# Optimization experiments

Measured on AMD Instinct MI355X. Metric: run time of the kernel, lower is better.

Reference implementation:

```python
import jax, jax.numpy as jnp
import numpy as np

B = 4096      # batch
D_IN = 512    # input_dim
D = 256       # d_model
T = 424       # n_targets
L = 6         # num_layers
EPS = 1e-5    # torch LayerNorm default


def _ln(x, g, b):
    m = jnp.mean(x, axis=-1, keepdims=True)
    v = jnp.var(x, axis=-1, keepdims=True)
    return (x - m) * jax.lax.rsqrt(v + EPS) * g + b


def setup_inputs() -> dict:
    key = jax.random.key(0)
    ks = iter(jax.random.split(key, 32))
    r = lambda shape, s=0.05: jax.random.normal(next(ks), shape, dtype=jnp.float32) * s
    return {
        'x': jax.random.normal(next(ks), (B, D_IN), dtype=jnp.float32),
        'proj_W': r((4, D // 4, D_IN)), 'proj_b': r((4, D // 4)),
        'attn_in_W': r((L, 3 * D, D)), 'attn_in_b': r((L, 3 * D)),
        'attn_out_W': r((L, D, D)), 'attn_out_b': r((L, D)),
        'ln_g': jnp.ones((L, D), jnp.float32), 'ln_b': jnp.zeros((L, D), jnp.float32),
        'ff_W1': r((L, 4 * D, D)), 'ff_b1': r((L, 4 * D)),
        'ff_W2': r((L, D, 4 * D)), 'ff_b2': r((L, D)),
        'cross_in_W': r((3 * D, D)), 'cross_in_b': r((3 * D,)),
        'cross_out_W': r((D, D)), 'cross_out_b': r((D,)),
        'tp_W1': r((T, D // 2, D)), 'tp_b1': r((T, D // 2)),
        'tp_ln_g': jnp.ones((T, D // 2), jnp.float32), 'tp_ln_b': jnp.zeros((T, D // 2), jnp.float32),
        'tp_W2': r((T, D // 4, D // 2)), 'tp_b2': r((T, D // 4)),
        'tp_W3': r((T, D // 4)), 'tp_b3': r((T,)),
    }


def reference(x, proj_W, proj_b, attn_in_W, attn_in_b, attn_out_W, attn_out_b,
              ln_g, ln_b, ff_W1, ff_b1, ff_W2, ff_b2,
              cross_in_W, cross_in_b, cross_out_W, cross_out_b,
              tp_W1, tp_b1, tp_ln_g, tp_ln_b, tp_W2, tp_b2, tp_W3, tp_b3):
    # 4 feature projections -> concat == reshape of stacked einsum  [B, 4, D/4] -> [B, D]
    h = jnp.einsum('bd,pkd->bpk', x, proj_W) + proj_b
    h = h.reshape(h.shape[0], D)

    # 6 transformer blocks on seq_len=1: softmax over a single key == 1, so
    # MHA(x,x,x) reduces exactly to out_proj(v_proj(x)); dropout = identity (eval).
    for i in range(L):
        Wv, bv = attn_in_W[i, 2 * D:], attn_in_b[i, 2 * D:]
        attn = (h @ Wv.T + bv) @ attn_out_W[i].T + attn_out_b[i]
        h = _ln(h + attn, ln_g[i], ln_b[i])          # same norm instance reused
        ff = jax.nn.gelu(h @ ff_W1[i].T + ff_b1[i], approximate=False) @ ff_W2[i].T + ff_b2[i]
        h = _ln(h + ff, ln_g[i], ln_b[i])

    # cross-target attention, also seq_len=1 -> v/out projections only
    Wv, bv = cross_in_W[2 * D:], cross_in_b[2 * D:]
    h = h + ((h @ Wv.T + bv) @ cross_out_W.T + cross_out_b)

    # 424 per-target MLP heads, batched as grouped GEMMs
    t = jnp.einsum('bd,tkd->btk', h, tp_W1) + tp_b1          # [B, T, 128]
    t = jax.nn.relu(_ln(t, tp_ln_g, tp_ln_b))
    t = jax.nn.relu(jnp.einsum('btk,tmk->btm', t, tp_W2) + tp_b2)  # [B, T, 64]
    out = jnp.einsum('btm,tm->bt', t, tp_W3) + tp_b3         # [B, T]
    return out
```

## Files before the change

kernel.cpp:

```cpp
#include <hip/hip_runtime.h>
#include <stdint.h>

using bf16x8 = __attribute__((ext_vector_type(8))) short;
using f32x4  = __attribute__((ext_vector_type(4))) float;

__device__ __forceinline__ f32x4 mfma16(bf16x8 a, bf16x8 b, f32x4 c) {
  return __builtin_amdgcn_mfma_f32_16x16x32_bf16(a, b, c, 0, 0, 0);
}

__device__ __forceinline__ unsigned short f2b_rne(float f) {
  union { float f; unsigned u; } v; v.f = f;
  unsigned r = v.u + 0x7fffu + ((v.u >> 16) & 1u);
  return (unsigned short)(r >> 16);
}

__device__ __forceinline__ void gload16(const void* g, void* l) {
  __builtin_amdgcn_global_load_lds(
      (const __attribute__((address_space(1))) void*)g,
      (__attribute__((address_space(3))) void*)l, 16, 0, 0);
}

__global__ void f2b_kernel(const float* __restrict__ s, unsigned short* __restrict__ d, int n4) {
  int i = blockIdx.x * 256 + threadIdx.x;
  if (i >= n4) return;
  float4 v = reinterpret_cast<const float4*>(s)[i];
  ushort4 o;
  o.x = f2b_rne(v.x); o.y = f2b_rne(v.y); o.z = f2b_rne(v.z); o.w = f2b_rne(v.w);
  reinterpret_cast<ushort4*>(d)[i] = o;
}

template<int EPI>
__global__ __launch_bounds__(256) void gemm_trunk(
    const unsigned short* __restrict__ A, const unsigned short* __restrict__ W,
    const float* __restrict__ bias, float* __restrict__ hf,
    unsigned short* __restrict__ ybf, const float* __restrict__ gam,
    const float* __restrict__ bet, int K, int Nout) {
  __shared__ char sm[34816];
  __shared__ float red[2][4][16];
  const int tid = threadIdx.x, wid = tid >> 6, lane = tid & 63;
  const int g = lane >> 4, r = lane & 15;
  const int row0 = blockIdx.x << 4;
  const int col0 = blockIdx.y << 8;

  f32x4 acc[4] = {};
  const int nk = K >> 5;

  for (int i = wid; i < 17; i += 4) {
    if (i < 16) gload16(W + (size_t)(col0 + i * 16 + (lane >> 2)) * K + (lane & 3) * 8,
                        sm + i * 1024);
    else        gload16(A + (size_t)(row0 + (lane >> 2)) * K + (lane & 3) * 8,
                        sm + 32768);
  }
  for (int ks = 0; ks < nk; ++ks) {
    const int buf = ks & 1;
    __syncthreads();
    if (ks + 1 < nk) {
      const int nb = buf ^ 1, k0 = (ks + 1) << 5;
      for (int i = wid; i < 17; i += 4) {
        if (i < 16) gload16(W + (size_t)(col0 + i * 16 + (lane >> 2)) * K + k0 + (lane & 3) * 8,
                            sm + nb * 16384 + i * 1024);
        else        gload16(A + (size_t)(row0 + (lane >> 2)) * K + k0 + (lane & 3) * 8,
                            sm + 32768 + nb * 1024);
      }
    }
    bf16x8 a = *reinterpret_cast<const bf16x8*>(sm + 32768 + buf * 1024 + r * 64 + g * 16);
#pragma unroll
    for (int n = 0; n < 4; ++n) {
      bf16x8 b = *reinterpret_cast<const bf16x8*>(sm + buf * 16384 + (wid * 64 + n * 16 + r) * 64 + g * 16);
      acc[n] = mfma16(a, b, acc[n]);
    }
  }

  if (EPI == 0 || EPI == 1) {
#pragma unroll
    for (int n = 0; n < 4; ++n) {
      const int lc = wid * 64 + n * 16 + r;
      const float bv = bias[col0 + lc];
#pragma unroll
      for (int j = 0; j < 4; ++j) {
        const int row = row0 + g * 4 + j;
        float y = acc[n][j] + bv;
        if (EPI == 1) y = 0.5f * y * (1.f + erff(y * 0.70710678118654752f));
        ybf[(size_t)row * Nout + col0 + lc] = f2b_rne(y);
      }
    }
  } else if (EPI == 2 || EPI == 4) {
#pragma unroll
    for (int n = 0; n < 4; ++n) {
      const int lc = wid * 64 + n * 16 + r;
      const float bv = bias[lc];
#pragma unroll
      for (int j = 0; j < 4; ++j) {
        const int row = row0 + g * 4 + j;
        float y = acc[n][j] + bv;
        if (EPI == 4) y += hf[(size_t)row * 256 + lc];
        hf[(size_t)row * 256 + lc]  = y;
        ybf[(size_t)row * 256 + lc] = f2b_rne(y);
      }
    }
  } else {
    float xx[4][4];
    float sum[4] = {0.f, 0.f, 0.f, 0.f}, sq[4] = {0.f, 0.f, 0.f, 0.f};
#pragma unroll
    for (int n = 0; n < 4; ++n) {
      const int lc = wid * 64 + n * 16 + r;
      const float bv = bias[lc];
#pragma unroll
      for (int j = 0; j < 4; ++j) {
        float v = hf[(size_t)(row0 + g * 4 + j) * 256 + lc] + acc[n][j] + bv;
        xx[n][j] = v; sum[j] += v; sq[j] += v * v;
      }
    }
#pragma unroll
    for (int m = 1; m < 16; m <<= 1) {
#pragma unroll
      for (int j = 0; j < 4; ++j) {
        sum[j] += __shfl_xor(sum[j], m, 64);
        sq[j]  += __shfl_xor(sq[j],  m, 64);
      }
    }
    if (r == 0) {
#pragma unroll
      for (int j = 0; j < 4; ++j) { red[0][wid][g * 4 + j] = sum[j]; red[1][wid][g * 4 + j] = sq[j]; }
    }
    __syncthreads();
    float mu[4], rs[4];
#pragma unroll
    for (int j = 0; j < 4; ++j) {
      float ts = red[0][0][g * 4 + j] + red[0][1][g * 4 + j] + red[0][2][g * 4 + j] + red[0][3][g * 4 + j];
      float tq = red[1][0][g * 4 + j] + red[1][1][g * 4 + j] + red[1][2][g * 4 + j] + red[1][3][g * 4 + j];
      float mean = ts * (1.f / 256.f);
      mu[j] = mean;
      rs[j] = rsqrtf(tq * (1.f / 256.f) - mean * mean + 1e-5f);
    }
#pragma unroll
    for (int n = 0; n < 4; ++n) {
      const int lc = wid * 64 + n * 16 + r;
      const float gm = gam[lc], bb = bet[lc];
#pragma unroll
      for (int j = 0; j < 4; ++j) {
        const int row = row0 + g * 4 + j;
        float y = (xx[n][j] - mu[j]) * rs[j] * gm + bb;
        hf[(size_t)row * 256 + lc]  = y;
        ybf[(size_t)row * 256 + lc] = f2b_rne(y);
      }
    }
  }
}

__global__ __launch_bounds__(512, 2) void phase_d2(
    const unsigned short* __restrict__ hbf, const unsigned short* __restrict__ w1b,
    const float* __restrict__ b1, const float* __restrict__ lng, const float* __restrict__ lnb,
    const unsigned short* __restrict__ w2b, const float* __restrict__ b2,
    const float* __restrict__ w3, const float* __restrict__ b3,
    float* __restrict__ out) {
  __shared__ char sm[149504];
  const int tid = threadIdx.x, wid = tid >> 6, lane = tid & 63;
  const int r = lane & 15, hi = lane >> 4;
  const int sw = (r & 7) << 4;
  const int t = blockIdx.y;

  const unsigned short* w1t = w1b + (size_t)t * 32768;
  const unsigned short* w2t = w2b + (size_t)t * 8192;
#pragma unroll
  for (int i = 0; i < 8; ++i) {
    const int id = tid + i * 512;
    const int c = id >> 5, s = id & 31;
    bf16x8 v = *reinterpret_cast<const bf16x8*>(w1t + c * 256 + s * 8);
    *reinterpret_cast<bf16x8*>(sm + c * 512 + ((s * 16) ^ ((c & 7) << 4))) = v;
  }
#pragma unroll
  for (int i = 0; i < 2; ++i) {
    const int id = tid + i * 512;
    const int c = id >> 4, s = id & 15;
    bf16x8 v = *reinterpret_cast<const bf16x8*>(w2t + c * 128 + s * 8);
    *reinterpret_cast<bf16x8*>(sm + 65536 + c * 256 + ((s * 16) ^ ((c & 7) << 4))) = v;
  }
  {
    float v;
    if (tid < 128)      v = b1 [t * 128 + tid];
    else if (tid < 256) v = lng[t * 128 + tid - 128];
    else if (tid < 384) v = lnb[t * 128 + tid - 256];
    else if (tid < 448) v = b2 [t * 64  + tid - 384];
    else                v = w3 [t * 64  + tid - 448];
    reinterpret_cast<float*>(sm + 81920)[tid] = v;
  }
  __syncthreads();

  const float* cb1 = reinterpret_cast<const float*>(sm + 81920);
  const float* cg  = cb1 + 128;
  const float* cbe = cb1 + 256;
  const float* cb2 = cb1 + 384;
  const float* cw3 = cb1 + 448;
  char* t1w = sm + 83968 + wid * 8192;
  const float b3t = b3[t];
  const int token_b0 = blockIdx.x * 1024;

  for (int tile = 0; tile < 2; ++tile) {
    const int B0 = token_b0 + tile * 512 + wid * 64;

    f32x4 acc1[8][4] = {};
    bf16x8 bc[4], bn[4];
#pragma unroll
    for (int bf = 0; bf < 4; ++bf)
      bc[bf] = *reinterpret_cast<const bf16x8*>(hbf + (size_t)(B0 + bf * 16 + r) * 256 + hi * 8);
#pragma unroll
    for (int ks = 0; ks < 8; ++ks) {
      bf16x8 a[8];
#pragma unroll
      for (int cf = 0; cf < 8; ++cf)
        a[cf] = *reinterpret_cast<const bf16x8*>(sm + (cf * 16 + r) * 512 + ((ks * 64 + hi * 16) ^ sw));
      if (ks < 7) {
#pragma unroll
        for (int bf = 0; bf < 4; ++bf)
          bn[bf] = *reinterpret_cast<const bf16x8*>(hbf + (size_t)(B0 + bf * 16 + r) * 256 + (ks + 1) * 32 + hi * 8);
      }
#pragma unroll
      for (int cf = 0; cf < 8; ++cf)
#pragma unroll
        for (int bf = 0; bf < 4; ++bf)
          acc1[cf][bf] = mfma16(a[cf], bc[bf], acc1[cf][bf]);
#pragma unroll
      for (int bf = 0; bf < 4; ++bf) bc[bf] = bn[bf];
    }

#pragma unroll
    for (int cf = 0; cf < 8; ++cf) {
      f32x4 b1v = *reinterpret_cast<const f32x4*>(cb1 + cf * 16 + hi * 4);
#pragma unroll
      for (int bf = 0; bf < 4; ++bf) acc1[cf][bf] += b1v;
    }

    float mu[4], rsd[4];
#pragma unroll
    for (int bf = 0; bf < 4; ++bf) {
      float s = 0.f, s2 = 0.f;
#pragma unroll
      for (int cf = 0; cf < 8; ++cf)
#pragma unroll
        for (int j = 0; j < 4; ++j) { float v = acc1[cf][bf][j]; s += v; s2 += v * v; }
      s  += __shfl_xor(s, 16, 64);  s  += __shfl_xor(s, 32, 64);
      s2 += __shfl_xor(s2, 16, 64); s2 += __shfl_xor(s2, 32, 64);
      const float m = s * (1.f / 128.f);
      mu[bf] = m;
      rsd[bf] = rsqrtf(s2 * (1.f / 128.f) - m * m + 1e-5f);
    }

    f32x4 acc2[4][4] = {};
#pragma unroll
    for (int half = 0; half < 2; ++half) {
#pragma unroll
      for (int cf = 0; cf < 8; ++cf) {
        f32x4 gv = *reinterpret_cast<const f32x4*>(cg  + cf * 16 + hi * 4);
        f32x4 bv = *reinterpret_cast<const f32x4*>(cbe + cf * 16 + hi * 4);
#pragma unroll
        for (int bl = 0; bl < 2; ++bl) {
          const int bf = half * 2 + bl;
          unsigned o01, o23;
          {
            float y0 = fmaxf((acc1[cf][bf][0] - mu[bf]) * rsd[bf] * gv[0] + bv[0], 0.f);
            float y1 = fmaxf((acc1[cf][bf][1] - mu[bf]) * rsd[bf] * gv[1] + bv[1], 0.f);
            float y2 = fmaxf((acc1[cf][bf][2] - mu[bf]) * rsd[bf] * gv[2] + bv[2], 0.f);
            float y3 = fmaxf((acc1[cf][bf][3] - mu[bf]) * rsd[bf] * gv[3] + bv[3], 0.f);
            o01 = (unsigned)f2b_rne(y0) | ((unsigned)f2b_rne(y1) << 16);
            o23 = (unsigned)f2b_rne(y2) | ((unsigned)f2b_rne(y3) << 16);
          }
          uint2 pk; pk.x = o01; pk.y = o23;
          *reinterpret_cast<uint2*>(t1w + (bl * 16 + r) * 256 + ((cf * 32 + hi * 8) ^ sw)) = pk;
        }
      }
#pragma unroll
      for (int ks = 0; ks < 4; ++ks) {
        bf16x8 a2[4];
#pragma unroll
        for (int cf2 = 0; cf2 < 4; ++cf2)
          a2[cf2] = *reinterpret_cast<const bf16x8*>(sm + 65536 + (cf2 * 16 + r) * 256 + ((ks * 64 + hi * 16) ^ sw));
#pragma unroll
        for (int bl = 0; bl < 2; ++bl) {
          bf16x8 bb = *reinterpret_cast<const bf16x8*>(t1w + (bl * 16 + r) * 256 + ((ks * 64 + hi * 16) ^ sw));
#pragma unroll
          for (int cf2 = 0; cf2 < 4; ++cf2)
            acc2[cf2][half * 2 + bl] = mfma16(a2[cf2], bb, acc2[cf2][half * 2 + bl]);
        }
      }
    }

    float s[4] = {0.f, 0.f, 0.f, 0.f};
#pragma unroll
    for (int cf2 = 0; cf2 < 4; ++cf2) {
      f32x4 b2v = *reinterpret_cast<const f32x4*>(cb2 + cf2 * 16 + hi * 4);
      f32x4 w3v = *reinterpret_cast<const f32x4*>(cw3 + cf2 * 16 + hi * 4);
#pragma unroll
      for (int bf = 0; bf < 4; ++bf)
#pragma unroll
        for (int j = 0; j < 4; ++j)
          s[bf] += fmaxf(acc2[cf2][bf][j] + b2v[j], 0.f) * w3v[j];
    }
#pragma unroll
    for (int bf = 0; bf < 4; ++bf) {
      s[bf] += __shfl_xor(s[bf], 16, 64);
      s[bf] += __shfl_xor(s[bf], 32, 64);
      if (hi == 0) out[(size_t)(B0 + bf * 16 + r) * 424 + t] = s[bf] + b3t;
    }
  }
}

extern "C" void kernel_launch(void* const* d_in, const int* in_sizes, int n_in,
                              void* d_out, int out_size, void* d_ws, size_t ws_size,
                              hipStream_t stream) {
  const float* x     = (const float*)d_in[0];
  const float* projW = (const float*)d_in[1];
  const float* projb = (const float*)d_in[2];
  const float* aiW   = (const float*)d_in[3];
  const float* aib   = (const float*)d_in[4];
  const float* aoW   = (const float*)d_in[5];
  const float* aob   = (const float*)d_in[6];
  const float* lng   = (const float*)d_in[7];
  const float* lnbp  = (const float*)d_in[8];
  const float* f1W   = (const float*)d_in[9];
  const float* f1b   = (const float*)d_in[10];
  const float* f2W   = (const float*)d_in[11];
  const float* f2bp  = (const float*)d_in[12];
  const float* ciW   = (const float*)d_in[13];
  const float* cib   = (const float*)d_in[14];
  const float* coW   = (const float*)d_in[15];
  const float* cob   = (const float*)d_in[16];
  const float* tpW1  = (const float*)d_in[17];
  const float* tpb1  = (const float*)d_in[18];
  const float* tplng = (const float*)d_in[19];
  const float* tplnb = (const float*)d_in[20];
  const float* tpW2  = (const float*)d_in[21];
  const float* tpb2  = (const float*)d_in[22];
  const float* tpW3  = (const float*)d_in[23];
  const float* tpb3  = (const float*)d_in[24];
  float* out = (float*)d_out;

  char* ws = (char*)d_ws;
  size_t off = 0;
  auto alloc = [&](size_t n) { char* p = ws + off; off = (off + n + 255) & ~(size_t)255; return p; };
  unsigned short* xb   = (unsigned short*)alloc(4096ull * 512 * 2);
  unsigned short* pWb  = (unsigned short*)alloc(256ull * 512 * 2);
  unsigned short* aiWb = (unsigned short*)alloc(6ull * 768 * 256 * 2);
  unsigned short* aoWb = (unsigned short*)alloc(6ull * 256 * 256 * 2);
  unsigned short* f1Wb = (unsigned short*)alloc(6ull * 1024 * 256 * 2);
  unsigned short* f2Wb = (unsigned short*)alloc(6ull * 256 * 1024 * 2);
  unsigned short* ciWb = (unsigned short*)alloc(768ull * 256 * 2);
  unsigned short* coWb = (unsigned short*)alloc(256ull * 256 * 2);
  unsigned short* W1b  = (unsigned short*)alloc(424ull * 128 * 256 * 2);
  unsigned short* W2b  = (unsigned short*)alloc(424ull * 64 * 128 * 2);
  float*          hf   = (float*)alloc(4096ull * 256 * 4);
  unsigned short* hbf  = (unsigned short*)alloc(4096ull * 256 * 2);
  unsigned short* vbf  = (unsigned short*)alloc(4096ull * 256 * 2);
  unsigned short* gbf  = (unsigned short*)alloc(4096ull * 1024 * 2);

  auto conv = [&](const float* s, unsigned short* d, size_t n) {
    int n4 = (int)(n >> 2);
    f2b_kernel<<<dim3((n4 + 255) / 256), dim3(256), 0, stream>>>(s, d, n4);
  };
  conv(x, xb, 4096ull * 512);
  conv(projW, pWb, 256ull * 512);
  conv(aiW, aiWb, 6ull * 768 * 256);
  conv(aoW, aoWb, 6ull * 256 * 256);
  conv(f1W, f1Wb, 6ull * 1024 * 256);
  conv(f2W, f2Wb, 6ull * 256 * 1024);
  conv(ciW, ciWb, 768ull * 256);
  conv(coW, coWb, 256ull * 256);
  conv(tpW1, W1b, 424ull * 128 * 256);
  conv(tpW2, W2b, 424ull * 64 * 128);

  dim3 blk(256);
  gemm_trunk<2><<<dim3(256, 1), blk, 0, stream>>>(xb, pWb, projb, hf, hbf, nullptr, nullptr, 512, 256);
  for (int i = 0; i < 6; ++i) {
    gemm_trunk<0><<<dim3(256, 1), blk, 0, stream>>>(hbf, aiWb + ((size_t)i * 768 + 512) * 256,
                                                    aib + i * 768 + 512, nullptr, vbf, nullptr, nullptr, 256, 256);
    gemm_trunk<3><<<dim3(256, 1), blk, 0, stream>>>(vbf, aoWb + (size_t)i * 256 * 256, aob + i * 256,
                                                    hf, hbf, lng + i * 256, lnbp + i * 256, 256, 256);
    gemm_trunk<1><<<dim3(256, 4), blk, 0, stream>>>(hbf, f1Wb + (size_t)i * 1024 * 256, f1b + i * 1024,
                                                    nullptr, gbf, nullptr, nullptr, 256, 1024);
    gemm_trunk<3><<<dim3(256, 1), blk, 0, stream>>>(gbf, f2Wb + (size_t)i * 256 * 1024, f2bp + i * 256,
                                                    hf, hbf, lng + i * 256, lnbp + i * 256, 1024, 256);
  }
  gemm_trunk<0><<<dim3(256, 1), blk, 0, stream>>>(hbf, ciWb + 512ull * 256, cib + 512,
                                                  nullptr, vbf, nullptr, nullptr, 256, 256);
  gemm_trunk<4><<<dim3(256, 1), blk, 0, stream>>>(vbf, coWb, cob, hf, hbf, nullptr, nullptr, 256, 256);

  phase_d2<<<dim3(4, 424), dim3(512), 0, stream>>>(hbf, W1b, tpb1, tplng, tplnb, W2b, tpb2, tpW3, tpb3, out);
}
```

Before: 599.4 us.

## Fold V and output projections into one weight, restructure trunk GEMM, add MFMA priority

Precomputes Wo·Wv and the combined bias for each attention block and for the cross block, so each of the seven V-projection plus out-projection GEMM pairs becomes a single GEMM and the vbf intermediate disappears. The trunk GEMM is rewritten to stage the A tile into swizzled LDS once and stream weights straight from global memory into registers, with templated row tiles and K. s_setprio is also wrapped around the MFMA bursts in the head kernel. The weight-composition kernel adds per-call fp32 work and rounds the product to bf16 once, which changes numerics slightly compared with rounding the two matrices separately.

```diff
diff --git a/kernel.cpp b/kernel.cpp
--- a/kernel.cpp
+++ b/kernel.cpp
@@ -12,12 +12,6 @@
   union { float f; unsigned u; } v; v.f = f;
   unsigned r = v.u + 0x7fffu + ((v.u >> 16) & 1u);
   return (unsigned short)(r >> 16);
-}
-
-__device__ __forceinline__ void gload16(const void* g, void* l) {
-  __builtin_amdgcn_global_load_lds(
-      (const __attribute__((address_space(1))) void*)g,
-      (__attribute__((address_space(3))) void*)l, 16, 0, 0);
 }
 
 __global__ void f2b_kernel(const float* __restrict__ s, unsigned short* __restrict__ d, int n4) {
@@ -29,86 +23,133 @@
   reinterpret_cast<ushort4*>(d)[i] = o;
 }
 
-template<int EPI>
-__global__ __launch_bounds__(256) void gemm_trunk(
+__global__ __launch_bounds__(256) void compose_attn(
+    const float* __restrict__ aiW, const float* __restrict__ aib,
+    const float* __restrict__ aoW, const float* __restrict__ aob,
+    const float* __restrict__ ciW, const float* __restrict__ cib,
+    const float* __restrict__ coW, const float* __restrict__ cob,
+    unsigned short* __restrict__ wEff, float* __restrict__ bEff) {
+  const int mat = blockIdx.y;
+  const float* Wo = (mat < 6) ? aoW + (size_t)mat * 65536 : coW;
+  const float* Wv = (mat < 6) ? aiW + (size_t)mat * 196608 + 131072 : ciW + 131072;
+  const float* bv = (mat < 6) ? aib + mat * 768 + 512 : cib + 512;
+  const float* bo = (mat < 6) ? aob + mat * 256 : cob;
+  unsigned short* Wd = wEff + (size_t)mat * 65536;
+  const int m = blockIdx.x * 16 + (threadIdx.x >> 4);
+  const int k0 = (threadIdx.x & 15) * 16;
+  float c[16] = {};
+  for (int j = 0; j < 256; ++j) {
+    const float a = Wo[m * 256 + j];
+    const float* Br = Wv + j * 256 + k0;
+#pragma unroll
+    for (int kk = 0; kk < 16; ++kk) c[kk] = fmaf(a, Br[kk], c[kk]);
+  }
+#pragma unroll
+  for (int kk = 0; kk < 16; ++kk) Wd[m * 256 + k0 + kk] = f2b_rne(c[kk]);
+  if (blockIdx.x == 0) {
+    const int mm = threadIdx.x;
+    float s = 0.f;
+    for (int j = 0; j < 256; ++j) s = fmaf(Wo[mm * 256 + j], bv[j], s);
+    bEff[mat * 256 + mm] = s + bo[mm];
+  }
+}
+
+template<int EPI, int ROWS, int K>
+__global__ __launch_bounds__(256, 4) void gemm_t2(
     const unsigned short* __restrict__ A, const unsigned short* __restrict__ W,
     const float* __restrict__ bias, float* __restrict__ hf,
     unsigned short* __restrict__ ybf, const float* __restrict__ gam,
-    const float* __restrict__ bet, int K, int Nout) {
-  __shared__ char sm[34816];
+    const float* __restrict__ bet, int Nout) {
+  constexpr int NBF = ROWS / 16;
+  constexpr int NCF = (ROWS == 16) ? 4 : 2;
+  constexpr int NK = K / 32;
+  constexpr int K2 = K * 2;
+  __shared__ char smA[ROWS * K2];
   __shared__ float red[2][4][16];
   const int tid = threadIdx.x, wid = tid >> 6, lane = tid & 63;
-  const int g = lane >> 4, r = lane & 15;
-  const int row0 = blockIdx.x << 4;
-  const int col0 = blockIdx.y << 8;
-
-  f32x4 acc[4] = {};
-  const int nk = K >> 5;
-
-  for (int i = wid; i < 17; i += 4) {
-    if (i < 16) gload16(W + (size_t)(col0 + i * 16 + (lane >> 2)) * K + (lane & 3) * 8,
-                        sm + i * 1024);
-    else        gload16(A + (size_t)(row0 + (lane >> 2)) * K + (lane & 3) * 8,
-                        sm + 32768);
-  }
-  for (int ks = 0; ks < nk; ++ks) {
-    const int buf = ks & 1;
-    __syncthreads();
-    if (ks + 1 < nk) {
-      const int nb = buf ^ 1, k0 = (ks + 1) << 5;
-      for (int i = wid; i < 17; i += 4) {
-        if (i < 16) gload16(W + (size_t)(col0 + i * 16 + (lane >> 2)) * K + k0 + (lane & 3) * 8,
-                            sm + nb * 16384 + i * 1024);
-        else        gload16(A + (size_t)(row0 + (lane >> 2)) * K + k0 + (lane & 3) * 8,
-                            sm + 32768 + nb * 1024);
-      }
-    }
-    bf16x8 a = *reinterpret_cast<const bf16x8*>(sm + 32768 + buf * 1024 + r * 64 + g * 16);
-#pragma unroll
-    for (int n = 0; n < 4; ++n) {
-      bf16x8 b = *reinterpret_cast<const bf16x8*>(sm + buf * 16384 + (wid * 64 + n * 16 + r) * 64 + g * 16);
-      acc[n] = mfma16(a, b, acc[n]);
-    }
-  }
-
-  if (EPI == 0 || EPI == 1) {
-#pragma unroll
-    for (int n = 0; n < 4; ++n) {
-      const int lc = wid * 64 + n * 16 + r;
-      const float bv = bias[col0 + lc];
-#pragma unroll
-      for (int j = 0; j < 4; ++j) {
-        const int row = row0 + g * 4 + j;
-        float y = acc[n][j] + bv;
-        if (EPI == 1) y = 0.5f * y * (1.f + erff(y * 0.70710678118654752f));
-        ybf[(size_t)row * Nout + col0 + lc] = f2b_rne(y);
-      }
-    }
+  const int r = lane & 15, hi = lane >> 4;
+  const int row0 = blockIdx.x * ROWS;
+  const int colW0 = ((ROWS == 16) ? 0 : blockIdx.y * 128) + wid * (NCF * 16);
+
+  constexpr int CHUNKS = ROWS * K / 8;
+  constexpr int CPR = K / 8;
+#pragma unroll
+  for (int id = tid; id < CHUNKS; id += 256) {
+    const int row = id / CPR, c8 = id % CPR;
+    bf16x8 v = *reinterpret_cast<const bf16x8*>(A + (size_t)(row0 + row) * K + c8 * 8);
+    *reinterpret_cast<bf16x8*>(smA + row * K2 + ((c8 * 16) ^ ((row & 7) << 4))) = v;
+  }
+  __syncthreads();
+
+  const unsigned short* Wb = W + (size_t)(colW0 + r) * K + hi * 8;
+  f32x4 acc[NBF][NCF] = {};
+  bf16x8 wc[NCF], wn[NCF];
+#pragma unroll
+  for (int cf = 0; cf < NCF; ++cf)
+    wc[cf] = *reinterpret_cast<const bf16x8*>(Wb + cf * 16 * K);
+#pragma unroll 4
+  for (int ks = 0; ks < NK; ++ks) {
+    if (ks + 1 < NK) {
+#pragma unroll
+      for (int cf = 0; cf < NCF; ++cf)
+        wn[cf] = *reinterpret_cast<const bf16x8*>(Wb + cf * 16 * K + (ks + 1) * 32);
+    }
+    bf16x8 av[NBF];
+#pragma unroll
+    for (int bf = 0; bf < NBF; ++bf)
+      av[bf] = *reinterpret_cast<const bf16x8*>(
+          smA + (bf * 16 + r) * K2 + ((ks * 64 + hi * 16) ^ ((r & 7) << 4)));
+#pragma unroll
+    for (int bf = 0; bf < NBF; ++bf)
+#pragma unroll
+      for (int cf = 0; cf < NCF; ++cf)
+        acc[bf][cf] = mfma16(av[bf], wc[cf], acc[bf][cf]);
+#pragma unroll
+    for (int cf = 0; cf < NCF; ++cf) wc[cf] = wn[cf];
+  }
+
+  if (EPI == 1) {
+#pragma unroll
+    for (int bf = 0; bf < NBF; ++bf)
+#pragma unroll
+      for (int cf = 0; cf < NCF; ++cf) {
+        const int col = colW0 + cf * 16 + r;
+        const float bv = bias[col];
+#pragma unroll
+        for (int j = 0; j < 4; ++j) {
+          const int row = row0 + bf * 16 + hi * 4 + j;
+          float y = acc[bf][cf][j] + bv;
+          y = 0.5f * y * (1.f + erff(y * 0.70710678118654752f));
+          ybf[(size_t)row * Nout + col] = f2b_rne(y);
+        }
+      }
   } else if (EPI == 2 || EPI == 4) {
 #pragma unroll
-    for (int n = 0; n < 4; ++n) {
-      const int lc = wid * 64 + n * 16 + r;
-      const float bv = bias[lc];
-#pragma unroll
-      for (int j = 0; j < 4; ++j) {
-        const int row = row0 + g * 4 + j;
-        float y = acc[n][j] + bv;
-        if (EPI == 4) y += hf[(size_t)row * 256 + lc];
-        hf[(size_t)row * 256 + lc]  = y;
-        ybf[(size_t)row * 256 + lc] = f2b_rne(y);
-      }
-    }
+    for (int bf = 0; bf < NBF; ++bf)
+#pragma unroll
+      for (int cf = 0; cf < NCF; ++cf) {
+        const int col = colW0 + cf * 16 + r;
+        const float bv = bias[col];
+#pragma unroll
+        for (int j = 0; j < 4; ++j) {
+          const int row = row0 + bf * 16 + hi * 4 + j;
+          float y = acc[bf][cf][j] + bv;
+          if (EPI == 4) y += hf[(size_t)row * 256 + col];
+          hf[(size_t)row * 256 + col]  = y;
+          ybf[(size_t)row * 256 + col] = f2b_rne(y);
+        }
+      }
   } else {
     float xx[4][4];
     float sum[4] = {0.f, 0.f, 0.f, 0.f}, sq[4] = {0.f, 0.f, 0.f, 0.f};
 #pragma unroll
-    for (int n = 0; n < 4; ++n) {
-      const int lc = wid * 64 + n * 16 + r;
-      const float bv = bias[lc];
+    for (int cf = 0; cf < 4; ++cf) {
+      const int col = colW0 + cf * 16 + r;
+      const float bv = bias[col];
 #pragma unroll
       for (int j = 0; j < 4; ++j) {
-        float v = hf[(size_t)(row0 + g * 4 + j) * 256 + lc] + acc[n][j] + bv;
-        xx[n][j] = v; sum[j] += v; sq[j] += v * v;
+        float v = hf[(size_t)(row0 + hi * 4 + j) * 256 + col] + acc[0][cf][j] + bv;
+        xx[cf][j] = v; sum[j] += v; sq[j] += v * v;
       }
     }
 #pragma unroll
@@ -121,28 +162,29 @@
     }
     if (r == 0) {
 #pragma unroll
-      for (int j = 0; j < 4; ++j) { red[0][wid][g * 4 + j] = sum[j]; red[1][wid][g * 4 + j] = sq[j]; }
+      for (int j = 0; j < 4; ++j) { red[0][wid][hi * 4 + j] = sum[j]; red[1][wid][hi * 4 + j] = sq[j]; }
     }
     __syncthreads();
     float mu[4], rs[4];
 #pragma unroll
     for (int j = 0; j < 4; ++j) {
-      float ts = red[0][0][g * 4 + j] + red[0][1][g * 4 + j] + red[0][2][g * 4 + j] + red[0][3][g * 4 + j];
-      float tq = red[1][0][g * 4 + j] + red[1][1][g * 4 + j] + red[1][2][g * 4 + j] + red[1][3][g * 4 + j];
+      const int rr = hi * 4 + j;
+      float ts = red[0][0][rr] + red[0][1][rr] + red[0][2][rr] + red[0][3][rr];
+      float tq = red[1][0][rr] + red[1][1][rr] + red[1][2][rr] + red[1][3][rr];
       float mean = ts * (1.f / 256.f);
       mu[j] = mean;
       rs[j] = rsqrtf(tq * (1.f / 256.f) - mean * mean + 1e-5f);
     }
 #pragma unroll
-    for (int n = 0; n < 4; ++n) {
-      const int lc = wid * 64 + n * 16 + r;
-      const float gm = gam[lc], bb = bet[lc];
+    for (int cf = 0; cf < 4; ++cf) {
+      const int col = colW0 + cf * 16 + r;
+      const float gm = gam[col], bb = bet[col];
 #pragma unroll
       for (int j = 0; j < 4; ++j) {
-        const int row = row0 + g * 4 + j;
-        float y = (xx[n][j] - mu[j]) * rs[j] * gm + bb;
-        hf[(size_t)row * 256 + lc]  = y;
-        ybf[(size_t)row * 256 + lc] = f2b_rne(y);
+        const int row = row0 + hi * 4 + j;
+        float y = (xx[cf][j] - mu[j]) * rs[j] * gm + bb;
+        hf[(size_t)row * 256 + col]  = y;
+        ybf[(size_t)row * 256 + col] = f2b_rne(y);
       }
     }
   }
@@ -215,11 +257,13 @@
         for (int bf = 0; bf < 4; ++bf)
           bn[bf] = *reinterpret_cast<const bf16x8*>(hbf + (size_t)(B0 + bf * 16 + r) * 256 + (ks + 1) * 32 + hi * 8);
       }
+      __builtin_amdgcn_s_setprio(1);
 #pragma unroll
       for (int cf = 0; cf < 8; ++cf)
 #pragma unroll
         for (int bf = 0; bf < 4; ++bf)
           acc1[cf][bf] = mfma16(a[cf], bc[bf], acc1[cf][bf]);
+      __builtin_amdgcn_s_setprio(0);
 #pragma unroll
       for (int bf = 0; bf < 4; ++bf) bc[bf] = bn[bf];
     }
@@ -275,6 +319,7 @@
 #pragma unroll
         for (int cf2 = 0; cf2 < 4; ++cf2)
           a2[cf2] = *reinterpret_cast<const bf16x8*>(sm + 65536 + (cf2 * 16 + r) * 256 + ((ks * 64 + hi * 16) ^ sw));
+        __builtin_amdgcn_s_setprio(1);
 #pragma unroll
         for (int bl = 0; bl < 2; ++bl) {
           bf16x8 bb = *reinterpret_cast<const bf16x8*>(t1w + (bl * 16 + r) * 256 + ((ks * 64 + hi * 16) ^ sw));
@@ -282,6 +327,7 @@
           for (int cf2 = 0; cf2 < 4; ++cf2)
             acc2[cf2][half * 2 + bl] = mfma16(a2[cf2], bb, acc2[cf2][half * 2 + bl]);
         }
+        __builtin_amdgcn_s_setprio(0);
       }
     }
 
@@ -340,49 +386,40 @@
   auto alloc = [&](size_t n) { char* p = ws + off; off = (off + n + 255) & ~(size_t)255; return p; };
   unsigned short* xb   = (unsigned short*)alloc(4096ull * 512 * 2);
   unsigned short* pWb  = (unsigned short*)alloc(256ull * 512 * 2);
-  unsigned short* aiWb = (unsigned short*)alloc(6ull * 768 * 256 * 2);
-  unsigned short* aoWb = (unsigned short*)alloc(6ull * 256 * 256 * 2);
   unsigned short* f1Wb = (unsigned short*)alloc(6ull * 1024 * 256 * 2);
   unsigned short* f2Wb = (unsigned short*)alloc(6ull * 256 * 1024 * 2);
-  unsigned short* ciWb = (unsigned short*)alloc(768ull * 256 * 2);
-  unsigned short* coWb = (unsigned short*)alloc(256ull * 256 * 2);
   unsigned short* W1b  = (unsigned short*)alloc(424ull * 128 * 256 * 2);
   unsigned short* W2b  = (unsigned short*)alloc(424ull * 64 * 128 * 2);
+  unsigned short* wEff = (unsigned short*)alloc(7ull * 256 * 256 * 2);
+  float*          bEff = (float*)alloc(7ull * 256 * 4);
   float*          hf   = (float*)alloc(4096ull * 256 * 4);
   unsigned short* hbf  = (unsigned short*)alloc(4096ull * 256 * 2);
-  unsigned short* vbf  = (unsigned short*)alloc(4096ull * 256 * 2);
   unsigned short* gbf  = (unsigned short*)alloc(4096ull * 1024 * 2);
 
   auto conv = [&](const float* s, unsigned short* d, size_t n) {
     int n4 = (int)(n >> 2);
     f2b_kernel<<<dim3((n4 + 255) / 256), dim3(256), 0, stream>>>(s, d, n4);
   };
+  compose_attn<<<dim3(16, 7), dim3(256), 0, stream>>>(aiW, aib, aoW, aob, ciW, cib, coW, cob, wEff, bEff);
   conv(x, xb, 4096ull * 512);
   conv(projW, pWb, 256ull * 512);
-  conv(aiW, aiWb, 6ull * 768 * 256);
-  conv(aoW, aoWb, 6ull * 256 * 256);
   conv(f1W, f1Wb, 6ull * 1024 * 256);
   conv(f2W, f2Wb, 6ull * 256 * 1024);
-  conv(ciW, ciWb, 768ull * 256);
-  conv(coW, coWb, 256ull * 256);
   conv(tpW1, W1b, 424ull * 128 * 256);
   conv(tpW2, W2b, 424ull * 64 * 128);
 
   dim3 blk(256);
-  gemm_trunk<2><<<dim3(256, 1), blk, 0, stream>>>(xb, pWb, projb, hf, hbf, nullptr, nullptr, 512, 256);
+  gemm_t2<2, 32, 512><<<dim3(128, 2), blk, 0, stream>>>(xb, pWb, projb, hf, hbf, nullptr, nullptr, 256);
   for (int i = 0; i < 6; ++i) {
-    gemm_trunk<0><<<dim3(256, 1), blk, 0, stream>>>(hbf, aiWb + ((size_t)i * 768 + 512) * 256,
-                                                    aib + i * 768 + 512, nullptr, vbf, nullptr, nullptr, 256, 256);
-    gemm_trunk<3><<<dim3(256, 1), blk, 0, stream>>>(vbf, aoWb + (size_t)i * 256 * 256, aob + i * 256,
-                                                    hf, hbf, lng + i * 256, lnbp + i * 256, 256, 256);
-    gemm_trunk<1><<<dim3(256, 4), blk, 0, stream>>>(hbf, f1Wb + (size_t)i * 1024 * 256, f1b + i * 1024,
-                                                    nullptr, gbf, nullptr, nullptr, 256, 1024);
-    gemm_trunk<3><<<dim3(256, 1), blk, 0, stream>>>(gbf, f2Wb + (size_t)i * 256 * 1024, f2bp + i * 256,
-                                                    hf, hbf, lng + i * 256, lnbp + i * 256, 1024, 256);
-  }
-  gemm_trunk<0><<<dim3(256, 1), blk, 0, stream>>>(hbf, ciWb + 512ull * 256, cib + 512,
-                                                  nullptr, vbf, nullptr, nullptr, 256, 256);
-  gemm_trunk<4><<<dim3(256, 1), blk, 0, stream>>>(vbf, coWb, cob, hf, hbf, nullptr, nullptr, 256, 256);
+    gemm_t2<3, 16, 256><<<dim3(256, 1), blk, 0, stream>>>(hbf, wEff + (size_t)i * 65536, bEff + i * 256,
+                                                          hf, hbf, lng + i * 256, lnbp + i * 256, 256);
+    gemm_t2<1, 32, 256><<<dim3(128, 8), blk, 0, stream>>>(hbf, f1Wb + (size_t)i * 1024 * 256, f1b + i * 1024,
+                                                          nullptr, gbf, nullptr, nullptr, 1024);
+    gemm_t2<3, 16, 1024><<<dim3(256, 1), blk, 0, stream>>>(gbf, f2Wb + (size_t)i * 256 * 1024, f2bp + i * 256,
+                                                           hf, hbf, lng + i * 256, lnbp + i * 256, 256);
+  }
+  gemm_t2<4, 32, 256><<<dim3(128, 2), blk, 0, stream>>>(hbf, wEff + 6ull * 65536, bEff + 6 * 256,
+                                                        hf, hbf, nullptr, nullptr, 256);
 
   phase_d2<<<dim3(4, 424), dim3(512), 0, stream>>>(hbf, W1b, tpb1, tplng, tplnb, W2b, tpb2, tpW3, tpb3, out);
 }
```

Result: slower. 621.8 us (+3.7%).
